# Performance work log

Measured on AMD Instinct MI355X. Metric: run time of the kernel, lower is better.

The kernel has to match this reference:

```python
import jax, jax.numpy as jnp
import numpy as np

SPATIAL_SHAPES = [(58, 100)]  # single level (H, W)
N_HEADS, N_LEVELS, N_POINTS, NUM_CAMS = 8, 1, 8, 6
D_MODEL = 256


def _bilinear_sample(v, loc, h, w):
    # v: (B, h, w, H, d); loc: (B, Lq, H, P, 2) normalized to [0,1]
    # matches F.grid_sample(mode='bilinear', padding_mode='zeros', align_corners=False)
    x = loc[..., 0] * w - 0.5
    y = loc[..., 1] * h - 0.5
    x0 = jnp.floor(x)
    y0 = jnp.floor(y)
    fx = x - x0
    fy = y - y0
    x0i = x0.astype(jnp.int32)
    y0i = y0.astype(jnp.int32)
    B, Hh = v.shape[0], v.shape[3]
    b = jnp.arange(B)[:, None, None, None]
    hd = jnp.arange(Hh)[None, None, :, None]

    def g(yi, xi):
        valid = ((yi >= 0) & (yi < h) & (xi >= 0) & (xi < w)).astype(v.dtype)
        yc = jnp.clip(yi, 0, h - 1)
        xc = jnp.clip(xi, 0, w - 1)
        return v[b, yc, xc, hd] * valid[..., None]  # (B,Lq,H,P,d)

    return (g(y0i, x0i) * ((1 - fy) * (1 - fx))[..., None]
            + g(y0i, x0i + 1) * ((1 - fy) * fx)[..., None]
            + g(y0i + 1, x0i) * (fy * (1 - fx))[..., None]
            + g(y0i + 1, x0i + 1) * (fy * fx)[..., None])


def _ms_deform_attn(value, locs, weights):
    # value: (B, S, H, d); locs: (B,Lq,H,L,P,2); weights: (B,Lq,H,L,P)
    B, S, Hh, d = value.shape
    out = 0.0
    start = 0
    for l, (h, w) in enumerate(SPATIAL_SHAPES):
        v = value[:, start:start + h * w].reshape(B, h, w, Hh, d)
        start += h * w
        samp = _bilinear_sample(v, locs[:, :, :, l], h, w)  # (B,Lq,H,P,d)
        out = out + jnp.einsum('bqhpd,bqhp->bqhd', samp, weights[:, :, :, l])
    return out.reshape(B, -1, Hh * d)


def setup_inputs() -> dict:
    key = jax.random.key(0)
    ks = jax.random.split(key, 12)
    B, Lq, C = 1, 22500, D_MODEL
    S = sum(h * w for h, w in SPATIAL_SHAPES)
    inp = {
        'query': jax.random.normal(ks[0], (B, Lq, C), jnp.float32),
        'reference_points_cam': jax.random.uniform(ks[1], (NUM_CAMS, B, Lq, 4, 2), jnp.float32),
        'bev_mask': jax.random.randint(ks[2], (NUM_CAMS, B, Lq, 4), 0, 2, jnp.int32),
        'value': jax.random.normal(ks[3], (B * NUM_CAMS, S, C), jnp.float32),
        'W_off': jax.random.normal(ks[4], (N_HEADS * N_LEVELS * N_POINTS * 2, C), jnp.float32) * 0.01,
        'b_off': jax.random.normal(ks[5], (N_HEADS * N_LEVELS * N_POINTS * 2,), jnp.float32),
        'W_attn': jax.random.normal(ks[6], (N_HEADS * N_LEVELS * N_POINTS, C), jnp.float32) * 0.02,
        'b_attn': jnp.zeros((N_HEADS * N_LEVELS * N_POINTS,), jnp.float32),
        'W_val': jax.random.normal(ks[7], (C, C), jnp.float32) * (1.0 / np.sqrt(C)),
        'b_val': jnp.zeros((C,), jnp.float32),
        'W_out': jax.random.normal(ks[8], (C, C), jnp.float32) * (1.0 / np.sqrt(C)),
        'b_out': jnp.zeros((C,), jnp.float32),
    }
    return inp


def reference(query, reference_points_cam, bev_mask, value,
              W_off, b_off, W_attn, b_attn, W_val, b_val, W_out, b_out):
    B, Lq, C = query.shape
    d = C // N_HEADS
    D = reference_points_cam.shape[3]  # num_Z_anchors = 4
    S = value.shape[1]

    # value_proj for all cameras; value rows are laid out as b*num_cams + cam
    val = value @ W_val.T + b_val
    val = val.reshape(B, NUM_CAMS, S, N_HEADS, d).transpose(1, 0, 2, 3, 4)  # (cams,B,S,H,d)

    # query-side projections are camera-independent
    off = (query @ W_off.T + b_off).reshape(B, Lq, N_HEADS, N_LEVELS, N_POINTS, 2)
    normalizer = jnp.array([[w, h] for (h, w) in SPATIAL_SHAPES], dtype=query.dtype)  # (L,2)
    off = off / normalizer[None, None, None, :, None, :]
    off = off.reshape(B, Lq, N_HEADS, N_LEVELS, N_POINTS // D, D, 2)

    aw = (query @ W_attn.T + b_attn).reshape(B, Lq, N_HEADS, N_LEVELS * N_POINTS)
    aw = jax.nn.softmax(aw, axis=-1).reshape(B, Lq, N_HEADS, N_LEVELS, N_POINTS)

    vis = (bev_mask.sum(-1) > 0)  # (cams, B, Lq)
    slots = jnp.zeros_like(query)
    for cam in range(NUM_CAMS):  # small fixed camera set
        ref = reference_points_cam[cam][:, :, None, None, None, :, :]  # (B,Lq,1,1,1,D,2)
        locs = (ref + off).reshape(B, Lq, N_HEADS, N_LEVELS, N_POINTS, 2)
        out = _ms_deform_attn(val[cam], locs, aw)  # (B,Lq,C)
        slots = slots + out * vis[cam][..., None].astype(query.dtype)

    count = jnp.maximum(vis.sum(0).astype(query.dtype), 1.0)  # (B,Lq)
    slots = slots / count[..., None]
    return slots @ W_out.T + b_out
```

## Files before the change

kernel.cpp:

```cpp
#include <hip/hip_runtime.h>

#define LQ     22500
#define SPA_H  58
#define SPA_W  100
#define S_TOT  5800
#define NCAMS  6
#define CDIM   256
#define NB_VAL 544
#define NB_Q   352
#define NB_VIS 88
#define NB_OUT 352

typedef __attribute__((ext_vector_type(8))) _Float16 half8;
typedef __attribute__((ext_vector_type(4))) float f32x4;

__device__ __forceinline__ half8 cvt_f32x8(const float* p) {
  f32x4 a = *(const f32x4*)p;
  f32x4 b = *(const f32x4*)(p + 4);
  half8 r;
  r[0] = (_Float16)a.x; r[1] = (_Float16)a.y; r[2] = (_Float16)a.z; r[3] = (_Float16)a.w;
  r[4] = (_Float16)b.x; r[5] = (_Float16)b.y; r[6] = (_Float16)b.z; r[7] = (_Float16)b.w;
  return r;
}

template<int N, int OUT_MODE, int BSEL, bool A_F16>
__device__ __forceinline__ void gemm_body(
    const void* __restrict__ Av, const float* __restrict__ W0,
    const float* __restrict__ W1, const float* __restrict__ b0,
    const float* __restrict__ b1, void* __restrict__ outA,
    float* __restrict__ outB, int M, int bid)
{
  constexpr int K  = CDIM;
  constexpr int NT = (N / 4) / 16;
  const int lane = threadIdx.x & 63;
  const int wave = threadIdx.x >> 6;
  const int m15  = lane & 15;
  const int quad = lane >> 4;
  const int rowbase = bid * 64;
  const int colbase = wave * (N / 4);

  const float* wp[NT];
  float bv[NT];
#pragma unroll
  for (int t = 0; t < NT; ++t) {
    const int c = colbase + t * 16 + m15;
    if (BSEL == 0) { wp[t] = W0 + (size_t)c * K; bv[t] = b0[c]; }
    else {
      wp[t] = (c < 128) ? (W0 + (size_t)c * K) : (W1 + (size_t)(c - 128) * K);
      bv[t] = (c < 128) ? b0[c] : b1[c - 128];
    }
  }

  f32x4 acc[4][NT];
#pragma unroll
  for (int rt = 0; rt < 4; ++rt)
#pragma unroll
    for (int t = 0; t < NT; ++t) acc[rt][t] = (f32x4){0.f, 0.f, 0.f, 0.f};

#pragma unroll
  for (int kk = 0; kk < K; kk += 32) {
    const int ko = kk + quad * 8;
    half8 a[4], b[NT];
#pragma unroll
    for (int rt = 0; rt < 4; ++rt) {
      int row = rowbase + rt * 16 + m15;
      row = row < M ? row : M - 1;
      if (A_F16) a[rt] = *(const half8*)((const _Float16*)Av + (size_t)row * K + ko);
      else       a[rt] = cvt_f32x8((const float*)Av + (size_t)row * K + ko);
    }
#pragma unroll
    for (int t = 0; t < NT; ++t) b[t] = cvt_f32x8(wp[t] + ko);
#pragma unroll
    for (int t = 0; t < NT; ++t)
#pragma unroll
      for (int rt = 0; rt < 4; ++rt)
        acc[rt][t] = __builtin_amdgcn_mfma_f32_16x16x32_f16(a[rt], b[t], acc[rt][t], 0, 0, 0);
  }

#pragma unroll
  for (int rt = 0; rt < 4; ++rt) {
    const int orow = rowbase + rt * 16 + quad * 4;
#pragma unroll
    for (int t = 0; t < NT; ++t) {
      const int col = colbase + t * 16 + m15;
      if (OUT_MODE == 3) {
        if (col >= 128) {
#pragma unroll
          for (int i = 0; i < 4; ++i) {
            const float v = acc[rt][t][i] + bv[t];
            float mx = v;
            mx = fmaxf(mx, __shfl_xor(mx, 1, 64));
            mx = fmaxf(mx, __shfl_xor(mx, 2, 64));
            mx = fmaxf(mx, __shfl_xor(mx, 4, 64));
            const float e = __expf(v - mx);
            float sm = e;
            sm += __shfl_xor(sm, 1, 64);
            sm += __shfl_xor(sm, 2, 64);
            sm += __shfl_xor(sm, 4, 64);
            const int r = orow + i;
            if (r < M) outB[(size_t)r * 64 + (col - 128)] = e / sm;
          }
        } else {
          const float sc = (col & 1) ? (1.f / SPA_H) : (1.f / SPA_W);
#pragma unroll
          for (int i = 0; i < 4; ++i) {
            const int r = orow + i;
            if (r < M)
              ((_Float16*)outA)[(size_t)r * 128 + col] =
                  (_Float16)((acc[rt][t][i] + bv[t]) * sc);
          }
        }
      } else {
#pragma unroll
        for (int i = 0; i < 4; ++i) {
          const int r = orow + i;
          if (r < M) {
            const float v = acc[rt][t][i] + bv[t];
            if (OUT_MODE == 0) ((float*)outA)[(size_t)r * N + col] = v;
            else               ((_Float16*)outA)[(size_t)r * N + col] = (_Float16)v;
          }
        }
      }
    }
  }
}

__device__ __forceinline__ void vis_body(const int* __restrict__ bev,
                                         unsigned char* __restrict__ vm,
                                         float* __restrict__ invc, int idx) {
  if (idx >= LQ) return;
  int cnt = 0; unsigned m = 0;
#pragma unroll
  for (int c = 0; c < NCAMS; ++c) {
    const int4 b4 = *(const int4*)(bev + ((size_t)c * LQ + idx) * 4);
    const int v = (b4.x + b4.y + b4.z + b4.w) > 0 ? 1 : 0;
    m |= (unsigned)v << c; cnt += v;
  }
  vm[idx] = (unsigned char)m;
  invc[idx] = 1.f / (float)(cnt > 0 ? cnt : 1);
}

__global__ __launch_bounds__(256, 2) void fused_front(
    const float* __restrict__ value, const float* __restrict__ query,
    const int* __restrict__ bev,
    const float* __restrict__ W_val, const float* __restrict__ b_val,
    const float* __restrict__ W_off, const float* __restrict__ b_off,
    const float* __restrict__ W_attn, const float* __restrict__ b_attn,
    _Float16* __restrict__ vp, _Float16* __restrict__ offb,
    float* __restrict__ wbuf, unsigned char* __restrict__ vm,
    float* __restrict__ invc) {
  const int bid = blockIdx.x;
  if (bid < NB_VAL)
    gemm_body<256, 2, 0, false>(value, W_val, nullptr, b_val, nullptr, vp,
                                nullptr, NCAMS * S_TOT, bid);
  else if (bid < NB_VAL + NB_Q)
    gemm_body<192, 3, 1, false>(query, W_off, W_attn, b_off, b_attn, offb,
                                wbuf, LQ, bid - NB_VAL);
  else
    vis_body(bev, vm, invc, (bid - NB_VAL - NB_Q) * 256 + (int)threadIdx.x);
}

__global__ __launch_bounds__(256, 2) void out_gemm(
    const _Float16* __restrict__ slots, const float* __restrict__ W_out,
    const float* __restrict__ b_out, float* __restrict__ out) {
  gemm_body<256, 0, 0, true>(slots, W_out, nullptr, b_out, nullptr, out,
                             nullptr, LQ, blockIdx.x);
}

__global__ __launch_bounds__(128) void sampler(
    const _Float16* __restrict__ vp,
    const _Float16* __restrict__ offb,
    const float* __restrict__ wbuf,
    const float* __restrict__ ref,
    const unsigned char* __restrict__ vm,
    const float* __restrict__ invc,
    _Float16* __restrict__ slots)
{
  const int t  = threadIdx.x;
  const int ql = t >> 4;
  const int s  = t & 15;
  const int h  = s >> 1;
  const int hf = s & 1;
  const int q  = blockIdx.x * 8 + ql;
  const bool qok = q < LQ;
  const int qc = qok ? q : LQ - 1;

  __shared__ float s_off[8][128];
  __shared__ float s_w[8][64];
  __shared__ float s_ref[8][48];
  __shared__ unsigned char s_vm[8];
  __shared__ float s_ic[8];

  {
    const half8 o8 = *(const half8*)(offb + (size_t)qc * 128 + s * 8);
#pragma unroll
    for (int k = 0; k < 8; ++k) s_off[ql][s * 8 + k] = (float)o8[k];
    const f32x4 w4 = *(const f32x4*)(wbuf + (size_t)qc * 64 + s * 4);
#pragma unroll
    for (int k = 0; k < 4; ++k) s_w[ql][s * 4 + k] = w4[k];
#pragma unroll
    for (int rep = 0; rep < 3; ++rep) {
      const int k = s + rep * 16;
      s_ref[ql][k] = ref[((size_t)(k >> 3) * LQ + qc) * 8 + (k & 7)];
    }
    if (s == 0) {
      s_vm[ql] = qok ? vm[q] : (unsigned char)0;
      s_ic[ql] = qok ? invc[q] : 1.f;
    }
  }
  __syncthreads();

  float w8[8], ox[8], oy[8];
#pragma unroll
  for (int p = 0; p < 8; ++p) {
    w8[p] = s_w[ql][h * 8 + p];
    ox[p] = s_off[ql][(h * 8 + p) * 2 + 0];
    oy[p] = s_off[ql][(h * 8 + p) * 2 + 1];
  }

  float acc[16];
#pragma unroll
  for (int i = 0; i < 16; ++i) acc[i] = 0.f;

  const int chbase = h * 32 + hf * 16;
  const unsigned vmq = s_vm[ql];

  for (int cam = 0; cam < NCAMS; ++cam) {
    if (!((vmq >> cam) & 1)) continue;
    const _Float16* vpc = vp + (size_t)cam * (S_TOT * CDIM) + chbase;
#pragma unroll
    for (int p = 0; p < 8; ++p) {
      const int z = p & 3;
      const float lx = s_ref[ql][cam * 8 + z * 2 + 0] + ox[p];
      const float ly = s_ref[ql][cam * 8 + z * 2 + 1] + oy[p];
      const float x = lx * 100.f - 0.5f;
      const float y = ly * 58.f - 0.5f;
      const float x0f = floorf(x), y0f = floorf(y);
      const float fx = x - x0f, fy = y - y0f;
      const int x0 = (int)x0f, y0 = (int)y0f;
      const float wgt = w8[p];
      const float w00 = (1.f - fy) * (1.f - fx) * wgt;
      const float w01 = (1.f - fy) * fx * wgt;
      const float w10 = fy * (1.f - fx) * wgt;
      const float w11 = fy * fx * wgt;
      const bool xv0 = (x0 >= 0) && (x0 < SPA_W);
      const bool xv1 = (x0 + 1 >= 0) && (x0 + 1 < SPA_W);
#pragma unroll
      for (int dy = 0; dy < 2; ++dy) {
        const int yy = y0 + dy;
        if (yy < 0 || yy >= SPA_H) continue;
        const _Float16* rowp = vpc + (size_t)(yy * SPA_W) * CDIM;
        const float wl = dy ? w10 : w00;
        const float wr = dy ? w11 : w01;
        if (xv0) {
          const _Float16* tp = rowp + (size_t)x0 * CDIM;
          half8 v0 = *(const half8*)tp;
          half8 v1 = *(const half8*)(tp + 8);
#pragma unroll
          for (int i = 0; i < 8; ++i) acc[i]     = fmaf(wl, (float)v0[i], acc[i]);
#pragma unroll
          for (int i = 0; i < 8; ++i) acc[8 + i] = fmaf(wl, (float)v1[i], acc[8 + i]);
        }
        if (xv1) {
          const _Float16* tp = rowp + (size_t)(x0 + 1) * CDIM;
          half8 v0 = *(const half8*)tp;
          half8 v1 = *(const half8*)(tp + 8);
#pragma unroll
          for (int i = 0; i < 8; ++i) acc[i]     = fmaf(wr, (float)v0[i], acc[i]);
#pragma unroll
          for (int i = 0; i < 8; ++i) acc[8 + i] = fmaf(wr, (float)v1[i], acc[8 + i]);
        }
      }
    }
  }

  if (qok) {
    const float sc = s_ic[ql];
    half8 o0, o1;
#pragma unroll
    for (int i = 0; i < 8; ++i) {
      o0[i] = (_Float16)(acc[i] * sc);
      o1[i] = (_Float16)(acc[8 + i] * sc);
    }
    _Float16* sp = slots + (size_t)q * CDIM + chbase;
    *(half8*)sp = o0;
    *(half8*)(sp + 8) = o1;
  }
}

extern "C" void kernel_launch(void* const* d_in, const int* in_sizes, int n_in,
                              void* d_out, int out_size, void* d_ws, size_t ws_size,
                              hipStream_t stream) {
  const float* query  = (const float*)d_in[0];
  const float* refpts = (const float*)d_in[1];
  const int*   bev    = (const int*)d_in[2];
  const float* value  = (const float*)d_in[3];
  const float* W_off  = (const float*)d_in[4];
  const float* b_off  = (const float*)d_in[5];
  const float* W_attn = (const float*)d_in[6];
  const float* b_attn = (const float*)d_in[7];
  const float* W_val  = (const float*)d_in[8];
  const float* b_val  = (const float*)d_in[9];
  const float* W_out  = (const float*)d_in[10];
  const float* b_out  = (const float*)d_in[11];

  char* ws = (char*)d_ws;
  _Float16*      vp    = (_Float16*)(ws + 0);
  _Float16*      offb  = (_Float16*)(ws + 17817600);
  float*         wbuf  = (float*)   (ws + 23577600);
  unsigned char* vm    = (unsigned char*)(ws + 29337600);
  float*         invc  = (float*)   (ws + 29360128);
  _Float16*      slots = (_Float16*)(ws + 29450128);

  fused_front<<<NB_VAL + NB_Q + NB_VIS, 256, 0, stream>>>(
      value, query, bev, W_val, b_val, W_off, b_off, W_attn, b_attn,
      vp, offb, wbuf, vm, invc);

  sampler<<<(LQ + 7) / 8, 128, 0, stream>>>(vp, offb, wbuf, refpts, vm, invc, slots);

  out_gemm<<<NB_OUT, 256, 0, stream>>>(slots, W_out, b_out, (float*)d_out);
}
```

Before: 415.9 us.

## Fuse output projection into sampler via shared-memory slots and MFMA epilogue

Drops the separate out_gemm launch and the global fp16 slots buffer. The sampler now handles 16 queries per 256-thread block, writes the normalized slot vectors to shared memory, and multiplies them by a pre-converted fp16 W_out with MFMA before writing fp32 outputs. W_out is converted to fp16 once in extra blocks of the front kernel. This removes a global round trip and a kernel launch, but every sampler block now re-reads the full 128 KB fp16 weight matrix and uses more shared memory, which may lower occupancy.

Result: no change. 412.2 us (-0.9%).

```diff
diff --git a/kernel.cpp b/kernel.cpp
--- a/kernel.cpp
+++ b/kernel.cpp
@@ -9,7 +9,8 @@
 #define NB_VAL 544
 #define NB_Q   352
 #define NB_VIS 88
-#define NB_OUT 352
+#define NB_CVT 32
+#define QPB    16
 
 typedef __attribute__((ext_vector_type(8))) _Float16 half8;
 typedef __attribute__((ext_vector_type(4))) float f32x4;
@@ -23,9 +24,9 @@
   return r;
 }
 
-template<int N, int OUT_MODE, int BSEL, bool A_F16>
+template<int N, int OUT_MODE, int BSEL>
 __device__ __forceinline__ void gemm_body(
-    const void* __restrict__ Av, const float* __restrict__ W0,
+    const float* __restrict__ A, const float* __restrict__ W0,
     const float* __restrict__ W1, const float* __restrict__ b0,
     const float* __restrict__ b1, void* __restrict__ outA,
     float* __restrict__ outB, int M, int bid)
@@ -65,8 +66,7 @@
     for (int rt = 0; rt < 4; ++rt) {
       int row = rowbase + rt * 16 + m15;
       row = row < M ? row : M - 1;
-      if (A_F16) a[rt] = *(const half8*)((const _Float16*)Av + (size_t)row * K + ko);
-      else       a[rt] = cvt_f32x8((const float*)Av + (size_t)row * K + ko);
+      a[rt] = cvt_f32x8(A + (size_t)row * K + ko);
     }
 #pragma unroll
     for (int t = 0; t < NT; ++t) b[t] = cvt_f32x8(wp[t] + ko);
@@ -114,11 +114,8 @@
 #pragma unroll
         for (int i = 0; i < 4; ++i) {
           const int r = orow + i;
-          if (r < M) {
-            const float v = acc[rt][t][i] + bv[t];
-            if (OUT_MODE == 0) ((float*)outA)[(size_t)r * N + col] = v;
-            else               ((_Float16*)outA)[(size_t)r * N + col] = (_Float16)v;
-          }
+          if (r < M)
+            ((_Float16*)outA)[(size_t)r * N + col] = (_Float16)(acc[rt][t][i] + bv[t]);
         }
       }
     }
@@ -146,50 +143,52 @@
     const float* __restrict__ W_val, const float* __restrict__ b_val,
     const float* __restrict__ W_off, const float* __restrict__ b_off,
     const float* __restrict__ W_attn, const float* __restrict__ b_attn,
+    const float* __restrict__ W_out,
     _Float16* __restrict__ vp, _Float16* __restrict__ offb,
     float* __restrict__ wbuf, unsigned char* __restrict__ vm,
-    float* __restrict__ invc) {
+    float* __restrict__ invc, _Float16* __restrict__ Wo_h) {
   const int bid = blockIdx.x;
   if (bid < NB_VAL)
-    gemm_body<256, 2, 0, false>(value, W_val, nullptr, b_val, nullptr, vp,
-                                nullptr, NCAMS * S_TOT, bid);
+    gemm_body<256, 2, 0>(value, W_val, nullptr, b_val, nullptr, vp,
+                         nullptr, NCAMS * S_TOT, bid);
   else if (bid < NB_VAL + NB_Q)
-    gemm_body<192, 3, 1, false>(query, W_off, W_attn, b_off, b_attn, offb,
-                                wbuf, LQ, bid - NB_VAL);
-  else
+    gemm_body<192, 3, 1>(query, W_off, W_attn, b_off, b_attn, offb,
+                         wbuf, LQ, bid - NB_VAL);
+  else if (bid < NB_VAL + NB_Q + NB_VIS)
     vis_body(bev, vm, invc, (bid - NB_VAL - NB_Q) * 256 + (int)threadIdx.x);
-}
-
-__global__ __launch_bounds__(256, 2) void out_gemm(
-    const _Float16* __restrict__ slots, const float* __restrict__ W_out,
-    const float* __restrict__ b_out, float* __restrict__ out) {
-  gemm_body<256, 0, 0, true>(slots, W_out, nullptr, b_out, nullptr, out,
-                             nullptr, LQ, blockIdx.x);
-}
-
-__global__ __launch_bounds__(128) void sampler(
+  else {
+    const int idx = (bid - NB_VAL - NB_Q - NB_VIS) * 2048 + (int)threadIdx.x * 8;
+    if (idx + 7 < 65536) *(half8*)(Wo_h + idx) = cvt_f32x8(W_out + idx);
+  }
+}
+
+#define SLOT_LD 280
+__global__ __launch_bounds__(256, 4) void sampler_out(
     const _Float16* __restrict__ vp,
     const _Float16* __restrict__ offb,
     const float* __restrict__ wbuf,
     const float* __restrict__ ref,
     const unsigned char* __restrict__ vm,
     const float* __restrict__ invc,
-    _Float16* __restrict__ slots)
+    const _Float16* __restrict__ Wo,
+    const float* __restrict__ b_out,
+    float* __restrict__ out)
 {
   const int t  = threadIdx.x;
   const int ql = t >> 4;
   const int s  = t & 15;
   const int h  = s >> 1;
   const int hf = s & 1;
-  const int q  = blockIdx.x * 8 + ql;
+  const int q  = blockIdx.x * QPB + ql;
   const bool qok = q < LQ;
   const int qc = qok ? q : LQ - 1;
 
-  __shared__ float s_off[8][128];
-  __shared__ float s_w[8][64];
-  __shared__ float s_ref[8][48];
-  __shared__ unsigned char s_vm[8];
-  __shared__ float s_ic[8];
+  __shared__ float s_off[QPB][128];
+  __shared__ float s_w[QPB][64];
+  __shared__ float s_ref[QPB][48];
+  __shared__ unsigned char s_vm[QPB];
+  __shared__ float s_ic[QPB];
+  __shared__ _Float16 s_slot[QPB][SLOT_LD];
 
   {
     const half8 o8 = *(const half8*)(offb + (size_t)qc * 128 + s * 8);
@@ -274,7 +273,7 @@
     }
   }
 
-  if (qok) {
+  {
     const float sc = s_ic[ql];
     half8 o0, o1;
 #pragma unroll
@@ -282,9 +281,50 @@
       o0[i] = (_Float16)(acc[i] * sc);
       o1[i] = (_Float16)(acc[8 + i] * sc);
     }
-    _Float16* sp = slots + (size_t)q * CDIM + chbase;
-    *(half8*)sp = o0;
-    *(half8*)(sp + 8) = o1;
+    *(half8*)&s_slot[ql][chbase] = o0;
+    *(half8*)&s_slot[ql][chbase + 8] = o1;
+  }
+  __syncthreads();
+
+  const int lane = t & 63;
+  const int wave = t >> 6;
+  const int m15  = lane & 15;
+  const int quad = lane >> 4;
+  const int colbase = wave * 64;
+
+  const _Float16* wrow[4];
+  float bvv[4];
+#pragma unroll
+  for (int tt = 0; tt < 4; ++tt) {
+    const int c = colbase + tt * 16 + m15;
+    wrow[tt] = Wo + (size_t)c * CDIM;
+    bvv[tt] = b_out[c];
+  }
+
+  f32x4 oacc[4];
+#pragma unroll
+  for (int tt = 0; tt < 4; ++tt) oacc[tt] = (f32x4){0.f, 0.f, 0.f, 0.f};
+
+#pragma unroll
+  for (int kk = 0; kk < CDIM; kk += 32) {
+    const int ko = kk + quad * 8;
+    const half8 a = *(const half8*)&s_slot[m15][ko];
+    half8 b[4];
+#pragma unroll
+    for (int tt = 0; tt < 4; ++tt) b[tt] = *(const half8*)(wrow[tt] + ko);
+#pragma unroll
+    for (int tt = 0; tt < 4; ++tt)
+      oacc[tt] = __builtin_amdgcn_mfma_f32_16x16x32_f16(a, b[tt], oacc[tt], 0, 0, 0);
+  }
+
+#pragma unroll
+  for (int tt = 0; tt < 4; ++tt) {
+    const int col = colbase + tt * 16 + m15;
+#pragma unroll
+    for (int i = 0; i < 4; ++i) {
+      const int r = blockIdx.x * QPB + quad * 4 + i;
+      if (r < LQ) out[(size_t)r * CDIM + col] = oacc[tt][i] + bvv[tt];
+    }
   }
 }
 
@@ -310,13 +350,12 @@
   float*         wbuf  = (float*)   (ws + 23577600);
   unsigned char* vm    = (unsigned char*)(ws + 29337600);
   float*         invc  = (float*)   (ws + 29360128);
-  _Float16*      slots = (_Float16*)(ws + 29450128);
-
-  fused_front<<<NB_VAL + NB_Q + NB_VIS, 256, 0, stream>>>(
-      value, query, bev, W_val, b_val, W_off, b_off, W_attn, b_attn,
-      vp, offb, wbuf, vm, invc);
-
-  sampler<<<(LQ + 7) / 8, 128, 0, stream>>>(vp, offb, wbuf, refpts, vm, invc, slots);
-
-  out_gemm<<<NB_OUT, 256, 0, stream>>>(slots, W_out, b_out, (float*)d_out);
-}
+  _Float16*      Wo_h  = (_Float16*)(ws + 29450240);
+
+  fused_front<<<NB_VAL + NB_Q + NB_VIS + NB_CVT, 256, 0, stream>>>(
+      value, query, bev, W_val, b_val, W_off, b_off, W_attn, b_attn, W_out,
+      vp, offb, wbuf, vm, invc, Wo_h);
+
+  sampler_out<<<(LQ + QPB - 1) / QPB, 256, 0, stream>>>(
+      vp, offb, wbuf, refpts, vm, invc, Wo_h, b_out, (float*)d_out);
+}
```
